# Kernel optimization log

Hardware: AMD Instinct MI355X
Metric: run time of the kernel (lower is better)

Reference implementation:

```python
import jax, jax.numpy as jnp
import numpy as np

MARGIN = 0.3
EPS = 1e-16


def _pairwise_distances(e):
    # e: [N, D] -> [N, N] euclidean distances (non-squared path)
    dot = jnp.matmul(e, e.T)
    sq = jnp.diagonal(dot)
    d = sq[None, :] + sq[:, None] - 2.0 * dot
    d = jnp.maximum(d, 0.0)
    zmask = (d == 0.0).astype(d.dtype)
    d = jnp.sqrt(d + zmask * EPS) * (1.0 - zmask)
    return d


def _masks(labels):
    n = labels.shape[0]
    eq = labels[None, :] == labels[:, None]          # [N, N]
    not_diag = ~jnp.eye(n, dtype=bool)
    ap_mask = eq & not_diag                          # anchor-positive
    an_mask = ~eq                                    # anchor-negative
    return ap_mask, an_mask


def _hard_loss(e, labels):
    d = _pairwise_distances(e)
    ap_mask, an_mask = _masks(labels)
    apf = ap_mask.astype(d.dtype)
    anf = an_mask.astype(d.dtype)
    hardest_pos = (apf * d).max(axis=1)
    max_d = d.max()
    hardest_neg = (d + max_d * (1.0 - anf)).min(axis=1)
    tl = jax.nn.relu(hardest_pos - hardest_neg + MARGIN)
    valid = apf.sum(axis=1) > 0
    cnt = valid.sum().astype(d.dtype)
    mean_loss = jnp.where(valid, tl, 0.0).sum() / jnp.maximum(cnt, 1.0)
    return jnp.where(cnt > 0, mean_loss, (e * 0).sum())


def _semi_hard_loss(e, labels):
    d = _pairwise_distances(e)                       # [N, N]
    ap_mask, an_mask = _masks(labels)
    ap = d[:, :, None]                               # [N, N, 1] anchor-positive dist
    an = d[:, None, :]                               # [N, 1, N] anchor-negative dist
    loss = ap - an + MARGIN                          # [N, N, N]
    valid = (ap_mask[:, :, None] & an_mask[:, None, :]
             & (an > ap) & (loss > 0))               # [N, N, N] bool
    num_valid = valid.sum()
    semi = (loss * valid.astype(loss.dtype)).sum() / jnp.maximum(
        num_valid.astype(loss.dtype), 1.0)
    return jnp.where(num_valid > 0, semi, _hard_loss(e, labels))


def setup_inputs() -> dict:
    key = jax.random.key(0)
    k1, k2 = jax.random.split(key)
    embeddings = jax.random.normal(k1, (384, 256), dtype=jnp.float32)
    labels = jax.random.randint(k2, (384,), 0, 32, dtype=jnp.int64)
    return {"embeddings": embeddings, "labels": labels}


def reference(embeddings, labels):
    return _semi_hard_loss(embeddings, labels)
```

## Files before the change

### kernel.cpp

```cpp
#include <hip/hip_runtime.h>
#include <math.h>

#define N 384
#define D 256
#define D4 (D/4)
#define TPB 256
#define MARGIN_F 0.3f

__global__ __launch_bounds__(TPB) void k_rows(const float* __restrict__ e,
                                              const int* __restrict__ labels,
                                              float* __restrict__ semi_sum,
                                              int* __restrict__ semi_cnt,
                                              float* __restrict__ hp_arr,
                                              float* __restrict__ mn_arr,
                                              float* __restrict__ rm_arr,
                                              int* __restrict__ pc_arr) {
  __shared__ float4 ei[D4];
  __shared__ float  row[N];
  __shared__ float  negd[N];
  __shared__ int    lab[N];
  __shared__ int    poslist[N];
  __shared__ int    npos;
  __shared__ float  w_s[4], w_hp[4], w_mn[4], w_rm[4];
  __shared__ int    w_c[4], w_pc[4];

  const int i = blockIdx.x;
  const int t = threadIdx.x;

  if (t < D4) ei[t] = ((const float4*)(e + (size_t)i * D))[t];
  lab[t] = labels[t];
  if (t < N - TPB) lab[t + TPB] = labels[t + TPB];
  if (t == 0) npos = 0;
  __syncthreads();

  const int li = lab[i];

  float l_hp = 0.0f;
  float l_mn = 1e30f;
  float l_rm = 0.0f;
  int   l_pc = 0;

  for (int j = t; j < N; j += TPB) {
    const float4* ej = (const float4*)(e + (size_t)j * D);
    float acc = 0.0f;
#pragma unroll 8
    for (int c = 0; c < D4; ++c) {
      float4 a = ei[c];
      float4 b = ej[c];
      float dx = a.x - b.x, dy = a.y - b.y, dz = a.z - b.z, dw = a.w - b.w;
      acc += dx * dx + dy * dy + dz * dz + dw * dw;
    }
    float dv = sqrtf(acc);
    row[j] = dv;
    bool eq    = (lab[j] == li);
    bool isneg = !eq;
    bool ispos = eq && (j != i);
    negd[j] = isneg ? dv : 1e30f;
    l_rm = fmaxf(l_rm, dv);
    if (isneg) l_mn = fminf(l_mn, dv);
    if (ispos) {
      l_hp = fmaxf(l_hp, dv);
      l_pc++;
      int idx = atomicAdd(&npos, 1);
      poslist[idx] = j;
    }
  }
  __syncthreads();

  float l_sum = 0.0f;
  int   l_cnt = 0;
  const int np = npos;
  for (int p = 0; p < np; ++p) {
    const float ap = row[poslist[p]];
    for (int k = t; k < N; k += TPB) {
      float an   = negd[k];
      float loss = ap - an + MARGIN_F;
      if (an > ap && loss > 0.0f) { l_sum += loss; l_cnt++; }
    }
  }

  for (int off = 32; off; off >>= 1) {
    l_sum += __shfl_down(l_sum, off);
    l_cnt += __shfl_down(l_cnt, off);
    l_hp = fmaxf(l_hp, __shfl_down(l_hp, off));
    l_mn = fminf(l_mn, __shfl_down(l_mn, off));
    l_rm = fmaxf(l_rm, __shfl_down(l_rm, off));
    l_pc += __shfl_down(l_pc, off);
  }
  const int wv = t >> 6;
  if ((t & 63) == 0) {
    w_s[wv] = l_sum; w_c[wv] = l_cnt; w_hp[wv] = l_hp;
    w_mn[wv] = l_mn; w_rm[wv] = l_rm; w_pc[wv] = l_pc;
  }
  __syncthreads();
  if (t == 0) {
    float S = 0.0f, HP = 0.0f, MN = 1e30f, RM = 0.0f;
    int C = 0, PC = 0;
    for (int w = 0; w < 4; ++w) {
      S += w_s[w]; C += w_c[w];
      HP = fmaxf(HP, w_hp[w]); MN = fminf(MN, w_mn[w]); RM = fmaxf(RM, w_rm[w]);
      PC += w_pc[w];
    }
    semi_sum[i] = S; semi_cnt[i] = C;
    hp_arr[i] = HP; mn_arr[i] = MN; rm_arr[i] = RM; pc_arr[i] = PC;
  }
}

__global__ __launch_bounds__(N) void k_final(const float* __restrict__ semi_sum,
                                             const int* __restrict__ semi_cnt,
                                             const float* __restrict__ hp_arr,
                                             const float* __restrict__ mn_arr,
                                             const float* __restrict__ rm_arr,
                                             const int* __restrict__ pc_arr,
                                             float* __restrict__ out) {
  const int t = threadIdx.x;
  __shared__ float shf[12];
  __shared__ int   shi[6];
  __shared__ float s_maxd, s_tsum;
  __shared__ int   s_tcnt;

  float s  = semi_sum[t];
  float rm = rm_arr[t];
  int   c  = semi_cnt[t];
  for (int off = 32; off; off >>= 1) {
    s += __shfl_down(s, off);
    rm = fmaxf(rm, __shfl_down(rm, off));
    c += __shfl_down(c, off);
  }
  const int wv = t >> 6;
  if ((t & 63) == 0) { shf[wv] = s; shf[6 + wv] = rm; shi[wv] = c; }
  __syncthreads();
  if (t == 0) {
    float ts = 0.0f, md = 0.0f; int tc = 0;
    for (int w = 0; w < 6; ++w) { ts += shf[w]; md = fmaxf(md, shf[6 + w]); tc += shi[w]; }
    s_tsum = ts; s_tcnt = tc; s_maxd = md;
  }
  __syncthreads();
  const float maxd = s_maxd;

  float hp  = hp_arr[t];
  float mnv = mn_arr[t];
  int   pcv = pc_arr[t];
  float hn  = fminf(mnv, maxd);
  float tl  = fmaxf(hp - hn + MARGIN_F, 0.0f);
  int   vld = (pcv > 0) ? 1 : 0;
  float contrib = vld ? tl : 0.0f;
  for (int off = 32; off; off >>= 1) {
    contrib += __shfl_down(contrib, off);
    vld += __shfl_down(vld, off);
  }
  __syncthreads();
  if ((t & 63) == 0) { shf[wv] = contrib; shi[wv] = vld; }
  __syncthreads();
  if (t == 0) {
    float hs = 0.0f; int vc = 0;
    for (int w = 0; w < 6; ++w) { hs += shf[w]; vc += shi[w]; }
    float semi = s_tsum / fmaxf((float)s_tcnt, 1.0f);
    float hard = (vc > 0) ? (hs / (float)vc) : 0.0f;
    out[0] = (s_tcnt > 0) ? semi : hard;
  }
}

extern "C" void kernel_launch(void* const* d_in, const int* in_sizes, int n_in,
                              void* d_out, int out_size, void* d_ws, size_t ws_size,
                              hipStream_t stream) {
  (void)in_sizes; (void)n_in; (void)out_size; (void)ws_size;
  const float* e      = (const float*)d_in[0];
  const int*   labels = (const int*)d_in[1];
  float*       out    = (float*)d_out;

  float* ws       = (float*)d_ws;
  float* semi_sum = ws;
  float* hp_arr   = ws + N;
  float* mn_arr   = ws + 2 * N;
  float* rm_arr   = ws + 3 * N;
  int*   semi_cnt = (int*)(ws + 4 * N);
  int*   pc_arr   = (int*)(ws + 5 * N);

  k_rows<<<N, TPB, 0, stream>>>(e, labels, semi_sum, semi_cnt,
                                hp_arr, mn_arr, rm_arr, pc_arr);
  k_final<<<1, N, 0, stream>>>(semi_sum, semi_cnt, hp_arr, mn_arr, rm_arr,
                               pc_arr, out);
}
```

Before: 83.78 us.

## Process three anchor rows per block using norm-based dot-product distances

Each block now handles three anchor rows with 384 threads, one per column j. Each thread streams its row of e once and computes the three dot products plus its own squared norm, which cuts the loads of the whole matrix from once per anchor to once per three anchors. Distances come from the norm-plus-dot formula like the reference. The semi-hard loop is reorganised so each thread owns one negative and loops over the positive list. The trade-offs are a grid of only 128 blocks, more registers per thread, and one thread per j reading a strided row, which gives uncoalesced global loads.

```diff
diff --git a/kernel.cpp b/kernel.cpp
--- a/kernel.cpp
+++ b/kernel.cpp
@@ -4,7 +4,10 @@
 #define N 384
 #define D 256
 #define D4 (D/4)
-#define TPB 256
+#define A 3
+#define GRID (N/A)
+#define TPB N
+#define NW (TPB/64)
 #define MARGIN_F 0.3f
 
 __global__ __launch_bounds__(TPB) void k_rows(const float* __restrict__ e,
@@ -15,94 +18,113 @@
                                               float* __restrict__ mn_arr,
                                               float* __restrict__ rm_arr,
                                               int* __restrict__ pc_arr) {
-  __shared__ float4 ei[D4];
-  __shared__ float  row[N];
-  __shared__ float  negd[N];
+  __shared__ float4 ei[A][D4];
+  __shared__ float  nrm[N];
+  __shared__ float  row[A][N];
+  __shared__ float  negd[A][N];
   __shared__ int    lab[N];
-  __shared__ int    poslist[N];
-  __shared__ int    npos;
-  __shared__ float  w_s[4], w_hp[4], w_mn[4], w_rm[4];
-  __shared__ int    w_c[4], w_pc[4];
-
-  const int i = blockIdx.x;
+  __shared__ int    poslist[A][N];
+  __shared__ int    npos[A];
+  __shared__ float  wredf[A][4][NW];
+  __shared__ int    wredi[A][2][NW];
+
+  const int b = blockIdx.x;
   const int t = threadIdx.x;
-
-  if (t < D4) ei[t] = ((const float4*)(e + (size_t)i * D))[t];
+  const int i0 = b * A;
+
   lab[t] = labels[t];
-  if (t < N - TPB) lab[t + TPB] = labels[t + TPB];
-  if (t == 0) npos = 0;
-  __syncthreads();
-
-  const int li = lab[i];
-
-  float l_hp = 0.0f;
-  float l_mn = 1e30f;
-  float l_rm = 0.0f;
-  int   l_pc = 0;
-
-  for (int j = t; j < N; j += TPB) {
-    const float4* ej = (const float4*)(e + (size_t)j * D);
-    float acc = 0.0f;
+  if (t < A * D4) {
+    int a = t / D4, c = t % D4;
+    ei[a][c] = ((const float4*)e)[(size_t)(i0 + a) * D4 + c];
+  }
+  if (t < A) npos[t] = 0;
+  __syncthreads();
+
+  const float4* ej = (const float4*)(e + (size_t)t * D);
+  float4 dv0 = {0,0,0,0}, dv1 = {0,0,0,0}, dv2 = {0,0,0,0}, nv = {0,0,0,0};
 #pragma unroll 8
-    for (int c = 0; c < D4; ++c) {
-      float4 a = ei[c];
-      float4 b = ej[c];
-      float dx = a.x - b.x, dy = a.y - b.y, dz = a.z - b.z, dw = a.w - b.w;
-      acc += dx * dx + dy * dy + dz * dz + dw * dw;
-    }
-    float dv = sqrtf(acc);
-    row[j] = dv;
-    bool eq    = (lab[j] == li);
-    bool isneg = !eq;
-    bool ispos = eq && (j != i);
-    negd[j] = isneg ? dv : 1e30f;
-    l_rm = fmaxf(l_rm, dv);
-    if (isneg) l_mn = fminf(l_mn, dv);
-    if (ispos) {
-      l_hp = fmaxf(l_hp, dv);
-      l_pc++;
-      int idx = atomicAdd(&npos, 1);
-      poslist[idx] = j;
-    }
-  }
-  __syncthreads();
-
-  float l_sum = 0.0f;
-  int   l_cnt = 0;
-  const int np = npos;
-  for (int p = 0; p < np; ++p) {
-    const float ap = row[poslist[p]];
-    for (int k = t; k < N; k += TPB) {
-      float an   = negd[k];
-      float loss = ap - an + MARGIN_F;
-      if (an > ap && loss > 0.0f) { l_sum += loss; l_cnt++; }
-    }
-  }
-
-  for (int off = 32; off; off >>= 1) {
-    l_sum += __shfl_down(l_sum, off);
-    l_cnt += __shfl_down(l_cnt, off);
-    l_hp = fmaxf(l_hp, __shfl_down(l_hp, off));
-    l_mn = fminf(l_mn, __shfl_down(l_mn, off));
-    l_rm = fmaxf(l_rm, __shfl_down(l_rm, off));
-    l_pc += __shfl_down(l_pc, off);
-  }
-  const int wv = t >> 6;
-  if ((t & 63) == 0) {
-    w_s[wv] = l_sum; w_c[wv] = l_cnt; w_hp[wv] = l_hp;
-    w_mn[wv] = l_mn; w_rm[wv] = l_rm; w_pc[wv] = l_pc;
-  }
-  __syncthreads();
-  if (t == 0) {
+  for (int c = 0; c < D4; ++c) {
+    float4 v = ej[c];
+    nv.x += v.x*v.x; nv.y += v.y*v.y; nv.z += v.z*v.z; nv.w += v.w*v.w;
+    float4 u0 = ei[0][c];
+    dv0.x += u0.x*v.x; dv0.y += u0.y*v.y; dv0.z += u0.z*v.z; dv0.w += u0.w*v.w;
+    float4 u1 = ei[1][c];
+    dv1.x += u1.x*v.x; dv1.y += u1.y*v.y; dv1.z += u1.z*v.z; dv1.w += u1.w*v.w;
+    float4 u2 = ei[2][c];
+    dv2.x += u2.x*v.x; dv2.y += u2.y*v.y; dv2.z += u2.z*v.z; dv2.w += u2.w*v.w;
+  }
+  const float nj = (nv.x + nv.y) + (nv.z + nv.w);
+  float dots[A];
+  dots[0] = (dv0.x + dv0.y) + (dv0.z + dv0.w);
+  dots[1] = (dv1.x + dv1.y) + (dv1.z + dv1.w);
+  dots[2] = (dv2.x + dv2.y) + (dv2.z + dv2.w);
+  nrm[t] = nj;
+  __syncthreads();
+
+  const int lj = lab[t];
+  float hpv[A], mnv[A], rmv[A];
+  int   pcv[A];
+#pragma unroll
+  for (int a = 0; a < A; ++a) {
+    const float ni = nrm[i0 + a];
+    float d2 = fmaxf(ni + nj - 2.0f * dots[a], 0.0f);
+    float dvv = (d2 > 0.0f) ? sqrtf(d2) : 0.0f;
+    const bool eq    = (lj == lab[i0 + a]);
+    const bool ispos = eq && (t != i0 + a);
+    row[a][t]  = dvv;
+    negd[a][t] = eq ? 1e30f : dvv;
+    rmv[a] = dvv;
+    mnv[a] = eq ? 1e30f : dvv;
+    hpv[a] = ispos ? dvv : 0.0f;
+    pcv[a] = ispos ? 1 : 0;
+    if (ispos) { int idx = atomicAdd(&npos[a], 1); poslist[a][idx] = t; }
+  }
+  __syncthreads();
+
+  const int w = t >> 6;
+#pragma unroll
+  for (int a = 0; a < A; ++a) {
+    const float an = negd[a][t];
+    float s = 0.0f;
+    int   c = 0;
+    const int np = npos[a];
+    for (int p = 0; p < np; ++p) {
+      const float ap = row[a][poslist[a][p]];
+      const float loss = ap - an + MARGIN_F;
+      if (an > ap && loss > 0.0f) { s += loss; c++; }
+    }
+    float hp = hpv[a], mn = mnv[a], rm = rmv[a];
+    int   pc = pcv[a];
+    for (int off = 32; off; off >>= 1) {
+      s  += __shfl_down(s, off);
+      c  += __shfl_down(c, off);
+      hp  = fmaxf(hp, __shfl_down(hp, off));
+      mn  = fminf(mn, __shfl_down(mn, off));
+      rm  = fmaxf(rm, __shfl_down(rm, off));
+      pc += __shfl_down(pc, off);
+    }
+    if ((t & 63) == 0) {
+      wredf[a][0][w] = s;  wredf[a][1][w] = hp;
+      wredf[a][2][w] = mn; wredf[a][3][w] = rm;
+      wredi[a][0][w] = c;  wredi[a][1][w] = pc;
+    }
+  }
+  __syncthreads();
+  if (t < A) {
     float S = 0.0f, HP = 0.0f, MN = 1e30f, RM = 0.0f;
-    int C = 0, PC = 0;
-    for (int w = 0; w < 4; ++w) {
-      S += w_s[w]; C += w_c[w];
-      HP = fmaxf(HP, w_hp[w]); MN = fminf(MN, w_mn[w]); RM = fmaxf(RM, w_rm[w]);
-      PC += w_pc[w];
-    }
+    int   C = 0, PC = 0;
+    for (int ww = 0; ww < NW; ++ww) {
+      S += wredf[t][0][ww];
+      HP = fmaxf(HP, wredf[t][1][ww]);
+      MN = fminf(MN, wredf[t][2][ww]);
+      RM = fmaxf(RM, wredf[t][3][ww]);
+      C += wredi[t][0][ww];
+      PC += wredi[t][1][ww];
+    }
+    const int i = i0 + t;
     semi_sum[i] = S; semi_cnt[i] = C;
-    hp_arr[i] = HP; mn_arr[i] = MN; rm_arr[i] = RM; pc_arr[i] = PC;
+    hp_arr[i] = HP;  mn_arr[i] = MN;
+    rm_arr[i] = RM;  pc_arr[i] = PC;
   }
 }
 
@@ -177,8 +199,8 @@
   int*   semi_cnt = (int*)(ws + 4 * N);
   int*   pc_arr   = (int*)(ws + 5 * N);
 
-  k_rows<<<N, TPB, 0, stream>>>(e, labels, semi_sum, semi_cnt,
-                                hp_arr, mn_arr, rm_arr, pc_arr);
+  k_rows<<<GRID, TPB, 0, stream>>>(e, labels, semi_sum, semi_cnt,
+                                   hp_arr, mn_arr, rm_arr, pc_arr);
   k_final<<<1, N, 0, stream>>>(semi_sum, semi_cnt, hp_arr, mn_arr, rm_arr,
                                pc_arr, out);
 }
```

New measurement: 73.90 us, median of 2. -11.8%, faster.
